# Performance work log

Measured on AMD Instinct MI355X. Metric: run time of the kernel, lower is better.

## Reference

```python
import jax, jax.numpy as jnp
import numpy as np

B, LQ, LK, D = 2, 2048, 2048, 1024
H, DK, DV = 16, 64, 64
EPS = 1e-6


def setup_inputs() -> dict:
    key = jax.random.key(0)
    ks = jax.random.split(key, 12)
    s = 1.0 / np.sqrt(D)
    return {
        "PE_states": jax.random.normal(ks[0], (B, LK, D), jnp.float32),
        "global_state": jax.random.normal(ks[1], (B, LQ, D), jnp.float32),
        "PE_statements": jax.random.normal(ks[2], (B, LK, D), jnp.float32),
        "PE_operators": jax.random.normal(ks[3], (B, LK, D), jnp.float32),
        "PE_solution_scores": jax.random.uniform(ks[4], (B, LK), jnp.float32),
        "mask": jax.random.randint(ks[5], (B, LQ, LK), 0, 2, jnp.int32),
        "w_q": jax.random.normal(ks[6], (D, H * DK), jnp.float32) * s,
        "w_k": jax.random.normal(ks[7], (D, H * DK), jnp.float32) * s,
        "w_v": jax.random.normal(ks[8], (D, H * DV), jnp.float32) * s,
        "w_fc": jax.random.normal(ks[9], (H * DV, D), jnp.float32) * s,
        "ln_gamma": jnp.ones((D,), jnp.float32),
        "ln_beta": jnp.zeros((D,), jnp.float32),
    }


def _layer_norm(x, gamma, beta):
    mu = jnp.mean(x, axis=-1, keepdims=True)
    var = jnp.mean(jnp.square(x - mu), axis=-1, keepdims=True)
    return (x - mu) * jax.lax.rsqrt(var + EPS) * gamma + beta


def reference(PE_states, global_state, PE_statements, PE_operators,
              PE_solution_scores, mask, w_q, w_k, w_v, w_fc, ln_gamma, ln_beta):
    # att_type == 'ca_sc', query_mode == 'PE', dropout == 0
    residual = global_state  # [B, LQ, D]
    q = (global_state @ w_q).reshape(B, LQ, H, DK).transpose(0, 2, 1, 3)   # bhqd
    k = (PE_states @ w_k).reshape(B, LK, H, DK).transpose(0, 2, 1, 3)      # bhkd
    v_s = (PE_statements @ w_v).reshape(B, LK, H, DV).transpose(0, 2, 1, 3)
    v_o = (PE_operators @ w_v).reshape(B, LK, H, DV).transpose(0, 2, 1, 3)

    temp = jnp.asarray(DK, jnp.float32) ** 0.5
    attn = jnp.einsum('bhqd,bhkd->bhqk', q / temp, k)  # [B,H,LQ,LK]
    # PE_solution_scores: per-key bias broadcast over heads and queries
    attn = (attn + PE_solution_scores[:, None, None, :]) / 2.0
    attn = jnp.where(mask[:, None, :, :] == 0, jnp.float32(-1e9), attn)
    attn = jax.nn.softmax(attn, axis=-1)

    def head_out(v):
        o = jnp.einsum('bhqk,bhkd->bhqd', attn, v)
        o = o.transpose(0, 2, 1, 3).reshape(B, LQ, H * DV)
        o = o @ w_fc + residual
        return _layer_norm(o, ln_gamma, ln_beta)

    statement_pred = head_out(v_s)
    operator_pred = head_out(v_o)
    return statement_pred, operator_pred
```

## Files before the change

kernel.cpp:

```cpp
#include <hip/hip_runtime.h>


typedef unsigned short u16;
typedef unsigned int   u32;
typedef unsigned long long u64;

typedef __attribute__((ext_vector_type(8))) short frag_ab;
typedef __attribute__((ext_vector_type(4))) float frag_cd;
typedef __attribute__((ext_vector_type(16))) float f32x16;
typedef __attribute__((ext_vector_type(8))) unsigned short u16x8;
typedef __attribute__((ext_vector_type(4))) unsigned short u16x4;
typedef __attribute__((ext_vector_type(2))) unsigned int u32x2;
typedef __attribute__((ext_vector_type(4))) int int4v;

__device__ __forceinline__ u16 f2bf(float f) {
    u32 x = __builtin_bit_cast(u32, f);
    return (u16)((x + 0x7fffu + ((x >> 16) & 1u)) >> 16);
}

__device__ __forceinline__ u32 pkbf(float a, float b) {
    return __builtin_amdgcn_perm(__builtin_bit_cast(u32, b),
                                 __builtin_bit_cast(u32, a), 0x07060302u);
}

#define GLDS16(gsrc, ldst)                                                     \
    __builtin_amdgcn_global_load_lds(                                          \
        (const __attribute__((address_space(1))) void*)(gsrc),                 \
        (__attribute__((address_space(3))) void*)(ldst), 16, 0, 0)

#define MFMA32(a, b, c) __builtin_amdgcn_mfma_f32_32x32x16_bf16(a, b, c, 0, 0, 0)

__global__ __launch_bounds__(256) void prep_kernel(
    const float* __restrict__ in0, const float* __restrict__ in1,
    const float* __restrict__ in2, const float* __restrict__ in3,
    u16* __restrict__ Ab4,
    const float* __restrict__ w_q, const float* __restrict__ w_k,
    const float* __restrict__ w_v, const float* __restrict__ w_fc,
    u16* __restrict__ wqT, u16* __restrict__ wkT,
    u16* __restrict__ wvT, u16* __restrict__ wfcT,
    const int* __restrict__ mask, u64* __restrict__ bits)
{
    __shared__ u16 tile[32][33];
    const int bid = blockIdx.x;
    const int tid = threadIdx.x;
    if (bid < 8192) {
        int z = bid >> 11;
        const float* in = z == 0 ? in0 : z == 1 ? in1 : z == 2 ? in2 : in3;
        u16* o = Ab4 + (size_t)z * 4194304;
        size_t i = ((size_t)(bid & 2047) * 256 + tid) * 8;
        float4 f0 = *(const float4*)(in + i);
        float4 f1 = *(const float4*)(in + i + 4);
        u16x8 t;
        t[0] = f2bf(f0.x); t[1] = f2bf(f0.y); t[2] = f2bf(f0.z); t[3] = f2bf(f0.w);
        t[4] = f2bf(f1.x); t[5] = f2bf(f1.y); t[6] = f2bf(f1.z); t[7] = f2bf(f1.w);
        *(u16x8*)(o + i) = t;
    } else if (bid < 12288) {
        int t = bid - 8192;
        int z = t >> 10;
        const float* in = z == 0 ? w_q : z == 1 ? w_k : z == 2 ? w_v : w_fc;
        u16* out = z == 0 ? wqT : z == 1 ? wkT : z == 2 ? wvT : wfcT;
        int bx = (t & 31) * 32, by = ((t >> 5) & 31) * 32;
        int tx = tid & 31, ty = tid >> 5;
        for (int i = 0; i < 32; i += 8)
            tile[ty + i][tx] = f2bf(in[(size_t)(by + ty + i) * 1024 + bx + tx]);
        __syncthreads();
        for (int i = 0; i < 32; i += 8)
            out[(size_t)(bx + ty + i) * 1024 + by + tx] = tile[tx][ty + i];
    } else {
        int pb = bid - 12288;
        int wv = tid >> 6, ln = tid & 63;
        long long base = (long long)pb * 2048 + wv * 512;
        for (int j = 0; j < 8; j++) {
            int v = mask[base + j * 64 + ln];
            u64 bl = __ballot(v != 0);
            if (ln == 0) bits[(base >> 6) + j] = bl;
        }
    }
}

__device__ __forceinline__ void gemm_core(
    const u16* __restrict__ A, const u16* __restrict__ BT,
    int bm, int bn, u16* Al, u16* Bl, frag_cd acc[4][4])
{
    const int tid = threadIdx.x;
    const int wave = tid >> 6, lane = tid & 63;
    const int ln15 = lane & 15, quad = lane >> 4;
    const int wm4 = (wave & 1) * 4, wn4 = (wave >> 1) * 4;

    for (int k0 = 0; k0 < 1024; k0 += 64) {
        for (int s = 0; s < 4; s++) {
            int f = wave * 4 + s;
            int grp = f >> 1, ks = f & 1;
            size_t col = k0 + ks * 32 + quad * 8;
            GLDS16(&A[(size_t)(bm + grp * 16 + ln15) * 1024 + col], Al + f * 512);
            GLDS16(&BT[(size_t)(bn + grp * 16 + ln15) * 1024 + col], Bl + f * 512);
        }
        __syncthreads();
        for (int ks = 0; ks < 2; ks++) {
            frag_ab a[4], b[4];
            for (int i = 0; i < 4; i++)
                a[i] = *(const frag_ab*)(Al + ((wm4 + i) * 2 + ks) * 512 + lane * 8);
            for (int j = 0; j < 4; j++)
                b[j] = *(const frag_ab*)(Bl + ((wn4 + j) * 2 + ks) * 512 + lane * 8);
            for (int i = 0; i < 4; i++)
                for (int j = 0; j < 4; j++)
                    acc[i][j] = __builtin_amdgcn_mfma_f32_16x16x32_bf16(a[i], b[j], acc[i][j], 0, 0, 0);
        }
        __syncthreads();
    }
}

__global__ __launch_bounds__(256, 4) void proj_gemm_kernel(
    const u16* __restrict__ Ab4,
    const u16* __restrict__ wqT, const u16* __restrict__ wkT, const u16* __restrict__ wvT,
    u16* __restrict__ Qb, u16* __restrict__ Kb,
    u16* __restrict__ VsT_g, u16* __restrict__ VoT_g)
{
    __shared__ alignas(16) u16 Al[16 * 512];
    __shared__ alignas(16) u16 Bl[16 * 512];
    const int z = blockIdx.z;
    const u16* A = Ab4 + (size_t)z * 4194304;
    const u16* BT = z == 0 ? wqT : z == 1 ? wkT : wvT;
    const int bm = blockIdx.x * 128, bn = blockIdx.y * 128;
    frag_cd acc[4][4] = {};
    gemm_core(A, BT, bm, bn, Al, Bl, acc);

    const int lane = threadIdx.x & 63;
    const int wave = threadIdx.x >> 6;
    const int ln15 = lane & 15, quad = lane >> 4;
    const int wm = (wave & 1) * 64, wn = (wave >> 1) * 64;
    if (z < 2) {
        u16* C = z == 0 ? Qb : Kb;
        const float qsc = z == 0 ? 0.09016844f : 1.0f;
        for (int i = 0; i < 4; i++) for (int j = 0; j < 4; j++) {
            int row0 = bm + wm + i * 16 + quad * 4;
            int col = bn + wn + j * 16 + ln15;
            for (int r = 0; r < 4; r++)
                C[(size_t)(row0 + r) * 1024 + col] = f2bf(acc[i][j][r] * qsc);
        }
    } else {
        u16* C = z == 2 ? VsT_g : VoT_g;
        for (int i = 0; i < 4; i++) for (int j = 0; j < 4; j++) {
            int row0 = bm + wm + i * 16 + quad * 4;
            int col = bn + wn + j * 16 + ln15;
            u16x4 t;
            for (int r = 0; r < 4; r++) t[r] = f2bf(acc[i][j][r]);
            *(u16x4*)&C[(size_t)col * 4096 + row0] = t;
        }
    }
}

__global__ __launch_bounds__(256, 3) void fc_gemm_kernel(
    const u16* __restrict__ Osb, const u16* __restrict__ Oob, const u16* __restrict__ wfcT,
    const float* __restrict__ resid, float* __restrict__ preLN)
{
    __shared__ alignas(16) u16 Al[16 * 512];
    __shared__ alignas(16) u16 Bl[16 * 512];
    const int z = blockIdx.z;
    const u16* A = z == 0 ? Osb : Oob;
    float* Cf = preLN + (size_t)z * 4194304;
    const int bm = blockIdx.x * 128, bn = blockIdx.y * 128;
    frag_cd acc[4][4] = {};
    gemm_core(A, wfcT, bm, bn, Al, Bl, acc);

    const int lane = threadIdx.x & 63;
    const int wave = threadIdx.x >> 6;
    const int ln15 = lane & 15, quad = lane >> 4;
    const int wm = (wave & 1) * 64, wn = (wave >> 1) * 64;
    for (int i = 0; i < 4; i++) for (int j = 0; j < 4; j++) {
        int row0 = bm + wm + i * 16 + quad * 4;
        int col = bn + wn + j * 16 + ln15;
        for (int r = 0; r < 4; r++) {
            size_t off = (size_t)(row0 + r) * 1024 + col;
            Cf[off] = acc[i][j][r] + resid[off];
        }
    }
}

__device__ __forceinline__ void flash_stage(
    const u16* __restrict__ Kp, const u16* __restrict__ VsT, const u16* __restrict__ VoT,
    int b, int h, int kt, int wave, int ln31, int hi, u16* buf)
{
    const int k0 = kt * 64;
    for (int s = 0; s < 6; s++) {
        int t = wave * 6 + s;
        const u16* g;
        if (t < 8) {
            int n = t >> 2, ks = t & 3;
            g = &Kp[(size_t)(b * 2048 + k0 + n * 32 + ln31) * 1024 + h * 64 + ks * 16 + hi * 8];
        } else if (t < 16) {
            int dt = (t >> 2) & 1, sk = t & 3;
            g = &VsT[(size_t)(h * 64 + dt * 32 + ln31) * 4096 + b * 2048 + k0 + sk * 16 + hi * 8];
        } else {
            int dt = (t >> 2) & 1, sk = t & 3;
            g = &VoT[(size_t)(h * 64 + dt * 32 + ln31) * 4096 + b * 2048 + k0 + sk * 16 + hi * 8];
        }
        GLDS16(g, buf + t * 512);
    }
}

__global__ __launch_bounds__(256, 2) void flash_kernel(
    const u16* __restrict__ Q, const u16* __restrict__ Kp,
    const u16* __restrict__ VsT_g, const u16* __restrict__ VoT_g,
    const float* __restrict__ scores, const u64* __restrict__ mbits,
    u16* __restrict__ Os, u16* __restrict__ Oo)
{
    __shared__ alignas(16) u16 KV[3][24 * 512];
    const int bid = blockIdx.x;
    const int xcd = bid & 7;
    const int qt = (bid >> 3) & 15;
    const int g = xcd + 8 * (bid >> 7);
    const int h = g & 15, b = g >> 4;
    const int tid = threadIdx.x;
    const int wave = tid >> 6, lane = tid & 63;
    const int ln31 = lane & 31, hi = lane >> 5;
    const int qbase = b * 2048 + qt * 128 + wave * 32;
    const int qrow = qbase + ln31;

    frag_ab aq0, aq1, aq2, aq3;
    {
        const u16* qp = &Q[(size_t)qrow * 1024 + h * 64 + hi * 8];
        aq0 = *(const frag_ab*)(qp);
        aq1 = *(const frag_ab*)(qp + 16);
        aq2 = *(const frag_ab*)(qp + 32);
        aq3 = *(const frag_ab*)(qp + 48);
    }
    frag_ab bbias = {};
    bbias[0] = (short)0x3F80; bbias[1] = (short)0x3F80;

    f32x16 os0 = {}, os1 = {}, oo0 = {}, oo1 = {};
    float l0 = 0.f, l1 = 0.f;
    const int shl4 = 4 - 4 * hi;

    auto softmax16 = [&](f32x16& s, u32 wa, float& lacc) {
#pragma unroll
        for (int r = 0; r < 16; r++) {
            const int bitc = (r & 3) + 8 * (r >> 2);
            u32 m = (u32)(((int)(wa << (27 - bitc))) >> 31);
            float e = __builtin_amdgcn_exp2f(s[r]);
            u32 pb = __builtin_bit_cast(u32, e) & m;
            float pf = __builtin_bit_cast(float, pb);
            lacc += pf;
            s[r] = pf;
        }
    };

    flash_stage(Kp, VsT_g, VoT_g, b, h, 0, wave, ln31, hi, KV[0]);
    flash_stage(Kp, VsT_g, VoT_g, b, h, 1, wave, ln31, hi, KV[1]);

    for (int kt = 0; kt < 32; kt++) {
        float sc0f = scores[b * 2048 + kt * 64 + ln31];
        float sc1f = scores[b * 2048 + kt * 64 + 32 + ln31];
        u64 w = mbits[(size_t)qrow * 32 + kt];
        if (kt < 31) asm volatile("s_waitcnt vmcnt(6) lgkmcnt(0)" ::: "memory");
        else         asm volatile("s_waitcnt vmcnt(0) lgkmcnt(0)" ::: "memory");
        __builtin_amdgcn_s_barrier();
        __builtin_amdgcn_sched_barrier(0);
        if (kt < 30)
            flash_stage(Kp, VsT_g, VoT_g, b, h, kt + 2, wave, ln31, hi, KV[(kt + 2) % 3]);
        const u16* bufp = KV[kt % 3];

        frag_ab ab0 = {}, ab1 = {};
        if (!hi) {
            float t0 = sc0f * 0.72134752f;
            u16 c0 = f2bf(t0);
            ab0[0] = (short)c0;
            ab0[1] = (short)f2bf(t0 - __builtin_bit_cast(float, (u32)c0 << 16));
            float t1 = sc1f * 0.72134752f;
            u16 c1 = f2bf(t1);
            ab1[0] = (short)c1;
            ab1[1] = (short)f2bf(t1 - __builtin_bit_cast(float, (u32)c1 << 16));
        }

        f32x16 sacc0 = {}, sacc1 = {};
        sacc0 = MFMA32(ab0, bbias, sacc0);
        sacc1 = MFMA32(ab1, bbias, sacc1);
#pragma unroll
        for (int ks = 0; ks < 4; ks++) {
            frag_ab ak0 = *(const frag_ab*)(bufp + (0 * 4 + ks) * 512 + lane * 8);
            frag_ab ak1 = *(const frag_ab*)(bufp + (1 * 4 + ks) * 512 + lane * 8);
            frag_ab q = ks == 0 ? aq0 : ks == 1 ? aq1 : ks == 2 ? aq2 : aq3;
            sacc0 = MFMA32(ak0, q, sacc0);
            sacc1 = MFMA32(ak1, q, sacc1);
        }

        u32 wa0 = ((u32)w) << shl4;
        u32 wa1 = ((u32)(w >> 32)) << shl4;
        softmax16(sacc0, wa0, l0);
        softmax16(sacc1, wa1, l1);

#pragma unroll
        for (int sk = 0; sk < 4; sk++) {
            const f32x16& ps = (sk < 2) ? sacc0 : sacc1;
            const int e0 = (sk & 1) * 8;
            u32 a0 = pkbf(ps[e0 + 0], ps[e0 + 1]);
            u32 a1 = pkbf(ps[e0 + 2], ps[e0 + 3]);
            u32 b0 = pkbf(ps[e0 + 4], ps[e0 + 5]);
            u32 b1 = pkbf(ps[e0 + 6], ps[e0 + 7]);
            u32x2 r0 = __builtin_amdgcn_permlane32_swap(a0, b0, false, false);
            u32x2 r1 = __builtin_amdgcn_permlane32_swap(a1, b1, false, false);
            int4v iv;
            iv[0] = (int)r0[0]; iv[1] = (int)r1[0];
            iv[2] = (int)r0[1]; iv[3] = (int)r1[1];
            frag_ab ap = __builtin_bit_cast(frag_ab, iv);
            frag_ab bs0 = *(const frag_ab*)(bufp + (8 + sk) * 512 + lane * 8);
            frag_ab bs1 = *(const frag_ab*)(bufp + (12 + sk) * 512 + lane * 8);
            frag_ab bo0 = *(const frag_ab*)(bufp + (16 + sk) * 512 + lane * 8);
            frag_ab bo1 = *(const frag_ab*)(bufp + (20 + sk) * 512 + lane * 8);
            os0 = MFMA32(ap, bs0, os0);
            os1 = MFMA32(ap, bs1, os1);
            oo0 = MFMA32(ap, bo0, oo0);
            oo1 = MFMA32(ap, bo1, oo1);
        }
    }

    float l_run = l0 + l1;
    float l_tot = l_run + __shfl_xor(l_run, 32, 64);
#pragma unroll
    for (int r = 0; r < 16; r++) {
        const int qr = (r & 3) + 8 * (r >> 2) + 4 * hi;
        float lv = __shfl(l_tot, qr, 64);
        float inv = 1.0f / fmaxf(lv, 1e-30f);
        size_t row = (size_t)(qbase + qr) * 1024 + h * 64;
        Os[row + ln31]      = f2bf(os0[r] * inv);
        Os[row + 32 + ln31] = f2bf(os1[r] * inv);
        Oo[row + ln31]      = f2bf(oo0[r] * inv);
        Oo[row + 32 + ln31] = f2bf(oo1[r] * inv);
    }
}

__global__ __launch_bounds__(256) void ln_kernel(
    const float* __restrict__ X, const float* __restrict__ gamma, const float* __restrict__ beta,
    float* __restrict__ out)
{
    __shared__ float red[4];
    int row = blockIdx.x;
    int tid = threadIdx.x;
    const float* x = X + (size_t)row * 1024;
    float4 v = *(const float4*)(x + tid * 4);
    float s = v.x + v.y + v.z + v.w;
    for (int off = 1; off < 64; off <<= 1) s += __shfl_xor(s, off, 64);
    int wv = tid >> 6, ln = tid & 63;
    if (ln == 0) red[wv] = s;
    __syncthreads();
    float mean = (red[0] + red[1] + red[2] + red[3]) * (1.0f / 1024.0f);
    float dx = v.x - mean, dy = v.y - mean, dz = v.z - mean, dw = v.w - mean;
    float s2 = dx * dx + dy * dy + dz * dz + dw * dw;
    for (int off = 1; off < 64; off <<= 1) s2 += __shfl_xor(s2, off, 64);
    __syncthreads();
    if (ln == 0) red[wv] = s2;
    __syncthreads();
    float var = (red[0] + red[1] + red[2] + red[3]) * (1.0f / 1024.0f);
    float rstd = rsqrtf(var + 1e-6f);
    float4 gg = *(const float4*)(gamma + tid * 4);
    float4 bb = *(const float4*)(beta + tid * 4);
    float4 o;
    o.x = dx * rstd * gg.x + bb.x;
    o.y = dy * rstd * gg.y + bb.y;
    o.z = dz * rstd * gg.z + bb.z;
    o.w = dw * rstd * gg.w + bb.w;
    *(float4*)(out + (size_t)row * 1024 + tid * 4) = o;
}

extern "C" void kernel_launch(void* const* d_in, const int* in_sizes, int n_in,
                              void* d_out, int out_size, void* d_ws, size_t ws_size,
                              hipStream_t stream)
{
    const float* PE_states     = (const float*)d_in[0];
    const float* global_state  = (const float*)d_in[1];
    const float* PE_statements = (const float*)d_in[2];
    const float* PE_operators  = (const float*)d_in[3];
    const float* scores        = (const float*)d_in[4];
    const int*   mask          = (const int*)d_in[5];
    const float* w_q  = (const float*)d_in[6];
    const float* w_k  = (const float*)d_in[7];
    const float* w_v  = (const float*)d_in[8];
    const float* w_fc = (const float*)d_in[9];
    const float* gamma = (const float*)d_in[10];
    const float* beta  = (const float*)d_in[11];
    float* out = (float*)d_out;

    char* ws = (char*)d_ws;
    const size_t MB = 1u << 20;
    u16* Ab4   = (u16*)(ws + 0 * MB);
    u16* Osb   = (u16*)(ws + 0 * MB);
    u16* Oob   = (u16*)(ws + 8 * MB);
    u16* wqT   = (u16*)(ws + 32 * MB);
    u16* wkT   = (u16*)(ws + 34 * MB);
    u16* wvT   = (u16*)(ws + 36 * MB);
    u16* wfcT  = (u16*)(ws + 38 * MB);
    u64* mbits = (u64*)(ws + 40 * MB);
    u16* Qb    = (u16*)(ws + 41 * MB);
    u16* Kb    = (u16*)(ws + 49 * MB);
    u16* VsT_g = (u16*)(ws + 57 * MB);
    u16* VoT_g = (u16*)(ws + 65 * MB);
    float* preLN = (float*)(ws + 41 * MB);

    prep_kernel<<<16384, 256, 0, stream>>>(
        global_state, PE_states, PE_statements, PE_operators, Ab4,
        w_q, w_k, w_v, w_fc, wqT, wkT, wvT, wfcT, mask, mbits);

    proj_gemm_kernel<<<dim3(32, 8, 4), 256, 0, stream>>>(
        Ab4, wqT, wkT, wvT, Qb, Kb, VsT_g, VoT_g);

    flash_kernel<<<dim3(512), 256, 0, stream>>>(Qb, Kb, VsT_g, VoT_g, scores, mbits, Osb, Oob);

    fc_gemm_kernel<<<dim3(32, 8, 2), 256, 0, stream>>>(Osb, Oob, wfcT, global_state, preLN);
    ln_kernel<<<8192, 256, 0, stream>>>(preLN, gamma, beta, out);
}
```

Baseline: 359.3 us.

## Use 256x256 tiled projection GEMM with 4-stage LDS ring; double-buffer flash

The projection GEMM moves from 128x128 tiles with 256 threads and a load-then-compute loop to 256x256 tiles with 512 threads. The new loop uses a 4-slot LDS ring with three stages prefetched ahead, manual waitcnt and barriers, and setprio around the MFMA groups. This aims to raise operand reuse per tile and hide global-to-LDS latency. The flash kernel separately drops from triple to double buffering, using __syncthreads and a one-stage prefetch. That cuts its LDS use but leaves less latency hiding. The 128KB ring per block and a grid of 256 blocks also limit occupancy to one block per CU.

```diff
diff --git a/kernel.cpp b/kernel.cpp
--- a/kernel.cpp
+++ b/kernel.cpp
@@ -78,6 +78,95 @@
     }
 }
 
+__device__ __forceinline__ void gemm256_core(
+    const u16* __restrict__ A, const u16* __restrict__ BT,
+    int bm, int bn, u16* ring, frag_cd acc[8][4])
+{
+    const int tid = threadIdx.x;
+    const int wave = tid >> 6, lane = tid & 63;
+    const int ln15 = lane & 15, quad = lane >> 4;
+    const int wr = wave >> 2, wc = wave & 3;
+
+    auto stage = [&](int t) {
+        u16* slot = ring + (t & 3) * 16384;
+        size_t col = (size_t)t * 32 + quad * 8;
+        for (int s = 0; s < 4; s++) {
+            int f = wave * 4 + s;
+            if (f < 16)
+                GLDS16(&A[(size_t)(bm + f * 16 + ln15) * 1024 + col], slot + f * 512);
+            else
+                GLDS16(&BT[(size_t)(bn + (f - 16) * 16 + ln15) * 1024 + col],
+                       slot + 8192 + (f - 16) * 512);
+        }
+    };
+
+    stage(0); stage(1); stage(2);
+
+    for (int t = 0; t < 32; t++) {
+        if (t < 30)       asm volatile("s_waitcnt vmcnt(8) lgkmcnt(0)" ::: "memory");
+        else if (t == 30) asm volatile("s_waitcnt vmcnt(4) lgkmcnt(0)" ::: "memory");
+        else              asm volatile("s_waitcnt vmcnt(0) lgkmcnt(0)" ::: "memory");
+        __builtin_amdgcn_s_barrier();
+        __builtin_amdgcn_sched_barrier(0);
+        if (t < 29) stage(t + 3);
+        const u16* slot = ring + (t & 3) * 16384;
+        const u16* aBase = slot + wr * 8 * 512;
+        const u16* bBase = slot + 8192 + wc * 4 * 512;
+        frag_ab b[4];
+#pragma unroll
+        for (int j = 0; j < 4; j++)
+            b[j] = *(const frag_ab*)(bBase + j * 512 + lane * 8);
+#pragma unroll
+        for (int m = 0; m < 8; m++) {
+            frag_ab a = *(const frag_ab*)(aBase + m * 512 + lane * 8);
+            __builtin_amdgcn_s_setprio(1);
+#pragma unroll
+            for (int j = 0; j < 4; j++)
+                acc[m][j] = __builtin_amdgcn_mfma_f32_16x16x32_bf16(a, b[j], acc[m][j], 0, 0, 0);
+            __builtin_amdgcn_s_setprio(0);
+        }
+    }
+}
+
+__global__ __launch_bounds__(512, 2) void proj_gemm_kernel(
+    const u16* __restrict__ Ab4,
+    const u16* __restrict__ wqT, const u16* __restrict__ wkT, const u16* __restrict__ wvT,
+    u16* __restrict__ Qb, u16* __restrict__ Kb,
+    u16* __restrict__ VsT_g, u16* __restrict__ VoT_g)
+{
+    __shared__ alignas(16) u16 ring[4 * 16384];
+    const int z = blockIdx.z;
+    const u16* A = Ab4 + (size_t)z * 4194304;
+    const u16* BT = z == 0 ? wqT : z == 1 ? wkT : wvT;
+    const int bm = blockIdx.x * 256, bn = blockIdx.y * 256;
+    frag_cd acc[8][4] = {};
+    gemm256_core(A, BT, bm, bn, ring, acc);
+
+    const int lane = threadIdx.x & 63;
+    const int wave = threadIdx.x >> 6;
+    const int ln15 = lane & 15, quad = lane >> 4;
+    const int wr = wave >> 2, wc = wave & 3;
+    if (z < 2) {
+        u16* C = z == 0 ? Qb : Kb;
+        const float qsc = z == 0 ? 0.09016844f : 1.0f;
+        for (int m = 0; m < 8; m++) for (int j = 0; j < 4; j++) {
+            int row0 = bm + wr * 128 + m * 16 + quad * 4;
+            int col = bn + wc * 64 + j * 16 + ln15;
+            for (int r = 0; r < 4; r++)
+                C[(size_t)(row0 + r) * 1024 + col] = f2bf(acc[m][j][r] * qsc);
+        }
+    } else {
+        u16* C = z == 2 ? VsT_g : VoT_g;
+        for (int m = 0; m < 8; m++) for (int j = 0; j < 4; j++) {
+            int row0 = bm + wr * 128 + m * 16 + quad * 4;
+            int col = bn + wc * 64 + j * 16 + ln15;
+            u16x4 t;
+            for (int r = 0; r < 4; r++) t[r] = f2bf(acc[m][j][r]);
+            *(u16x4*)&C[(size_t)col * 4096 + row0] = t;
+        }
+    }
+}
+
 __device__ __forceinline__ void gemm_core(
     const u16* __restrict__ A, const u16* __restrict__ BT,
     int bm, int bn, u16* Al, u16* Bl, frag_cd acc[4][4])
@@ -107,46 +196,6 @@
                     acc[i][j] = __builtin_amdgcn_mfma_f32_16x16x32_bf16(a[i], b[j], acc[i][j], 0, 0, 0);
         }
         __syncthreads();
-    }
-}
-
-__global__ __launch_bounds__(256, 4) void proj_gemm_kernel(
-    const u16* __restrict__ Ab4,
-    const u16* __restrict__ wqT, const u16* __restrict__ wkT, const u16* __restrict__ wvT,
-    u16* __restrict__ Qb, u16* __restrict__ Kb,
-    u16* __restrict__ VsT_g, u16* __restrict__ VoT_g)
-{
-    __shared__ alignas(16) u16 Al[16 * 512];
-    __shared__ alignas(16) u16 Bl[16 * 512];
-    const int z = blockIdx.z;
-    const u16* A = Ab4 + (size_t)z * 4194304;
-    const u16* BT = z == 0 ? wqT : z == 1 ? wkT : wvT;
-    const int bm = blockIdx.x * 128, bn = blockIdx.y * 128;
-    frag_cd acc[4][4] = {};
-    gemm_core(A, BT, bm, bn, Al, Bl, acc);
-
-    const int lane = threadIdx.x & 63;
-    const int wave = threadIdx.x >> 6;
-    const int ln15 = lane & 15, quad = lane >> 4;
-    const int wm = (wave & 1) * 64, wn = (wave >> 1) * 64;
-    if (z < 2) {
-        u16* C = z == 0 ? Qb : Kb;
-        const float qsc = z == 0 ? 0.09016844f : 1.0f;
-        for (int i = 0; i < 4; i++) for (int j = 0; j < 4; j++) {
-            int row0 = bm + wm + i * 16 + quad * 4;
-            int col = bn + wn + j * 16 + ln15;
-            for (int r = 0; r < 4; r++)
-                C[(size_t)(row0 + r) * 1024 + col] = f2bf(acc[i][j][r] * qsc);
-        }
-    } else {
-        u16* C = z == 2 ? VsT_g : VoT_g;
-        for (int i = 0; i < 4; i++) for (int j = 0; j < 4; j++) {
-            int row0 = bm + wm + i * 16 + quad * 4;
-            int col = bn + wn + j * 16 + ln15;
-            u16x4 t;
-            for (int r = 0; r < 4; r++) t[r] = f2bf(acc[i][j][r]);
-            *(u16x4*)&C[(size_t)col * 4096 + row0] = t;
-        }
     }
 }
 
@@ -205,7 +254,7 @@
     const float* __restrict__ scores, const u64* __restrict__ mbits,
     u16* __restrict__ Os, u16* __restrict__ Oo)
 {
-    __shared__ alignas(16) u16 KV[3][24 * 512];
+    __shared__ alignas(16) u16 KV[2][24 * 512];
     const int bid = blockIdx.x;
     const int xcd = bid & 7;
     const int qt = (bid >> 3) & 15;
@@ -246,19 +295,16 @@
     };
 
     flash_stage(Kp, VsT_g, VoT_g, b, h, 0, wave, ln31, hi, KV[0]);
-    flash_stage(Kp, VsT_g, VoT_g, b, h, 1, wave, ln31, hi, KV[1]);
 
     for (int kt = 0; kt < 32; kt++) {
+        const int p = kt & 1;
         float sc0f = scores[b * 2048 + kt * 64 + ln31];
         float sc1f = scores[b * 2048 + kt * 64 + 32 + ln31];
         u64 w = mbits[(size_t)qrow * 32 + kt];
-        if (kt < 31) asm volatile("s_waitcnt vmcnt(6) lgkmcnt(0)" ::: "memory");
-        else         asm volatile("s_waitcnt vmcnt(0) lgkmcnt(0)" ::: "memory");
-        __builtin_amdgcn_s_barrier();
-        __builtin_amdgcn_sched_barrier(0);
-        if (kt < 30)
-            flash_stage(Kp, VsT_g, VoT_g, b, h, kt + 2, wave, ln31, hi, KV[(kt + 2) % 3]);
-        const u16* bufp = KV[kt % 3];
+        __syncthreads();
+        if (kt < 31)
+            flash_stage(Kp, VsT_g, VoT_g, b, h, kt + 1, wave, ln31, hi, KV[p ^ 1]);
+        const u16* bufp = KV[p];
 
         frag_ab ab0 = {}, ab1 = {};
         if (!hi) {
@@ -400,7 +446,7 @@
         global_state, PE_states, PE_statements, PE_operators, Ab4,
         w_q, w_k, w_v, w_fc, wqT, wkT, wvT, wfcT, mask, mbits);
 
-    proj_gemm_kernel<<<dim3(32, 8, 4), 256, 0, stream>>>(
+    proj_gemm_kernel<<<dim3(16, 4, 4), 512, 0, stream>>>(
         Ab4, wqT, wkT, wvT, Qb, Kb, VsT_g, VoT_g);
 
     flash_kernel<<<dim3(512), 256, 0, stream>>>(Qb, Kb, VsT_g, VoT_g, scores, mbits, Osb, Oob);
```

New measurement: 330.2 us. -8.1%, faster.
